# Kernel optimization log

Hardware: AMD Instinct MI355X
Metric: run time of the kernel (lower is better)

The kernel has to match this reference:

```python
import jax, jax.numpy as jnp
import numpy as np
import math

B, S, HID = 2, 4096, 2048
H, D, C = 16, 128, 256  # heads, head_dim, chunk (block) size
NC = S // C


def _build_slopes(n):
    # faithful port of MiniMaxText01LinearAttention._build_slope_tensor
    def p2(m):
        start = 2.0 ** (-(2.0 ** (-(math.log2(m) - 3))))
        return [start * (start ** i) for i in range(m)]
    if math.log2(n).is_integer():
        sl = p2(n)
    else:
        cp = 2 ** math.floor(math.log2(n))
        sl = p2(cp) + p2(2 * cp)[0::2][: n - cp]
    return np.asarray(sl, dtype=np.float32).reshape(n, 1, 1)


def setup_inputs() -> dict:
    key = jax.random.key(0)
    k1, k2, k3, k4 = jax.random.split(key, 4)
    x = jax.random.normal(k1, (B, S, HID), dtype=jnp.float32)
    w_qkv = jax.random.normal(k2, (HID, 3 * H * D), dtype=jnp.float32) * 0.02
    w_gate = jax.random.normal(k3, (HID, H * D), dtype=jnp.float32) * 0.02
    w_out = jax.random.normal(k4, (H * D, HID), dtype=jnp.float32) * 0.02
    slopes = jnp.asarray(_build_slopes(H))  # [H,1,1]
    return {"x": x, "w_qkv": w_qkv, "w_gate": w_gate, "w_out": w_out, "slopes": slopes}


def _to_chunks(t):
    # [B,S,H*D] -> [NC,B,H,C,D]
    return (t.reshape(B, S, H, D)
             .transpose(0, 2, 1, 3)          # [B,H,S,D]
             .reshape(B, H, NC, C, D)
             .transpose(2, 0, 1, 3, 4))      # [NC,B,H,C,D]


def _lightning_attn(q, k, v, slopes):
    # q,k,v: [NC,B,H,C,D]; slopes: [H,1,1]
    s = slopes
    pos = jnp.arange(C, dtype=jnp.float32)
    q_decay = jnp.exp(-s * (pos + 1.0).reshape(1, C, 1))        # [H,C,1]
    k_decay = jnp.exp(-s * (C - 1.0 - pos).reshape(1, C, 1))    # [H,C,1]
    idx = pos[:, None] - pos[None, :]                            # [C,C]
    diag_decay = jnp.where(idx >= 0, jnp.exp(-s * idx), 0.0)     # [H,C,C]
    block_decay = jnp.exp(-s * float(C))[None]                   # [1,H,1,1]

    def step(kv, qkv_c):
        qc, kc, vc = qkv_c  # each [B,H,C,D]
        # intra-chunk (causal, decayed)
        scores = jnp.einsum('bhid,bhjd->bhij', qc, kc) * diag_decay
        o = jnp.einsum('bhij,bhjd->bhid', scores, vc)
        # inter-chunk via recurrent state kv: [B,H,D,D]
        o = o + jnp.einsum('bhid,bhde->bhie', qc * q_decay, kv)
        kv = block_decay * kv + jnp.einsum('bhjd,bhje->bhde', kc * k_decay, vc)
        return kv, o

    kv0 = jnp.zeros((B, H, D, D), dtype=q.dtype)
    _, outs = jax.lax.scan(step, kv0, (q, k, v))  # outs: [NC,B,H,C,D]
    return (outs.transpose(1, 2, 0, 3, 4)          # [B,H,NC,C,D]
                .reshape(B, H, S, D)
                .transpose(0, 2, 1, 3)
                .reshape(B, S, H * D))


def reference(x, w_qkv, w_gate, w_out, slopes):
    qkv = jax.nn.silu(x @ w_qkv)                   # act on fused qkv (hidden_act=silu)
    q, k, v = jnp.split(qkv, 3, axis=-1)
    attn = _lightning_attn(_to_chunks(q), _to_chunks(k), _to_chunks(v), slopes)
    gate = jax.nn.sigmoid(x @ w_gate)              # output gate
    return (gate * attn) @ w_out
```

## Files before the change

kernel.cpp:

```cpp
#include <hip/hip_runtime.h>

typedef __bf16 bf16;
typedef __bf16 bf16x8 __attribute__((ext_vector_type(8)));
typedef __bf16 bf16x4 __attribute__((ext_vector_type(4)));
typedef float  f32x4  __attribute__((ext_vector_type(4)));

#define B_   2
#define S_   4096
#define HID_ 2048
#define H_   16
#define D_   128
#define C_   256
#define NC_  16
#define M_   (B_*S_)
#define K_   2048

typedef __attribute__((address_space(1))) const void gas_t;
typedef __attribute__((address_space(3))) void las_t;

__global__ void cvt_kernel(const float* __restrict__ x,
                           const float* __restrict__ wqkv,
                           const float* __restrict__ wgate,
                           const float* __restrict__ wout,
                           bf16* __restrict__ xb, bf16* __restrict__ wT) {
    __shared__ float tile[32][33];
    int bid = blockIdx.x, tid = threadIdx.x;
    if (bid < 8192) {
        int idx = (bid * 256 + tid) * 8;
        float4 f0 = *(const float4*)(x + idx);
        float4 f1 = *(const float4*)(x + idx + 4);
        bf16x8 o;
        o[0] = (bf16)f0.x; o[1] = (bf16)f0.y; o[2] = (bf16)f0.z; o[3] = (bf16)f0.w;
        o[4] = (bf16)f1.x; o[5] = (bf16)f1.y; o[6] = (bf16)f1.z; o[7] = (bf16)f1.w;
        *(bf16x8*)(xb + idx) = o;
        return;
    }
    bid -= 8192;
    int k0 = (bid & 63) * 32, n0 = (bid >> 6) * 32;
    const float* src; int ld, col0;
    if (n0 < 6144)      { src = wqkv;  ld = 6144; col0 = n0; }
    else if (n0 < 8192) { src = wgate; ld = 2048; col0 = n0 - 6144; }
    else                { src = wout;  ld = 2048; col0 = n0 - 8192; }
    int tx = tid & 31, ty = tid >> 5;
#pragma unroll
    for (int i = 0; i < 4; i++) {
        int kk = ty + i * 8;
        tile[kk][tx] = src[(size_t)(k0 + kk) * ld + col0 + tx];
    }
    __syncthreads();
#pragma unroll
    for (int i = 0; i < 4; i++) {
        int nn = ty + i * 8;
        wT[(size_t)(n0 + nn) * K_ + k0 + tx] = (bf16)tile[tx][nn];
    }
}

template <int MODE>
__global__ __launch_bounds__(256) void gemm_kernel(
        const bf16* __restrict__ A, const bf16* __restrict__ Bm,
        bf16* __restrict__ qo, bf16* __restrict__ ko,
        bf16* __restrict__ vo, bf16* __restrict__ go,
        float* __restrict__ out) {
    __shared__ __align__(16) bf16 As[128 * 64];
    __shared__ __align__(16) bf16 Bs[128 * 64];
    const int m0 = blockIdx.x * 128, n0 = blockIdx.y * 128;
    const int tid = threadIdx.x, lane = tid & 63, wid = tid >> 6;
    const int quad = lane >> 4, l15 = lane & 15;
    const int i0w = (wid >> 1) * 64, j0w = (wid & 1) * 64;
    f32x4 acc[4][4] = {};
    const int srow = tid >> 3;
    const int sl = (tid & 7) ^ (srow & 7);
    const bf16* Ag = A  + (size_t)(m0 + srow) * K_ + sl * 8;
    const bf16* Bg = Bm + (size_t)(n0 + srow) * K_ + sl * 8;
    bf16* AsDst = As + tid * 8;
    bf16* BsDst = Bs + tid * 8;
    const int xr = l15 & 7;

    for (int kb = 0; kb < K_; kb += 64) {
#pragma unroll
        for (int r = 0; r < 4; r++) {
            __builtin_amdgcn_global_load_lds((gas_t*)(Ag + kb + (size_t)r * 32 * K_),
                                             (las_t*)(AsDst + r * 2048), 16, 0, 0);
            __builtin_amdgcn_global_load_lds((gas_t*)(Bg + kb + (size_t)r * 32 * K_),
                                             (las_t*)(BsDst + r * 2048), 16, 0, 0);
        }
        __syncthreads();
        bf16x8 af[2][4], bfr[2][4];
#pragma unroll
        for (int s2 = 0; s2 < 2; s2++) {
            const int slot = (s2 * 4 + quad) ^ xr;
#pragma unroll
            for (int t = 0; t < 4; t++) {
                af[s2][t]  = *(const bf16x8*)&As[(i0w + t * 16 + l15) * 64 + slot * 8];
                bfr[s2][t] = *(const bf16x8*)&Bs[(j0w + t * 16 + l15) * 64 + slot * 8];
            }
        }
#pragma unroll
        for (int s2 = 0; s2 < 2; s2++)
#pragma unroll
            for (int ti = 0; ti < 4; ti++)
#pragma unroll
                for (int tj = 0; tj < 4; tj++)
                    acc[ti][tj] = __builtin_amdgcn_mfma_f32_16x16x32_bf16(
                        af[s2][ti], bfr[s2][tj], acc[ti][tj], 0, 0, 0);
        __syncthreads();
    }

    if (MODE == 0) {
        bf16* outb = (n0 < 2048) ? qo : (n0 < 4096) ? ko : (n0 < 6144) ? vo : go;
        const bool silu = (n0 < 6144);
        const int cb = n0 & 2047;
#pragma unroll
        for (int ti = 0; ti < 4; ti++)
#pragma unroll
            for (int tj = 0; tj < 4; tj++)
#pragma unroll
                for (int r = 0; r < 4; r++) {
                    int row = m0 + i0w + ti * 16 + quad * 4 + r;
                    int col = cb + j0w + tj * 16 + l15;
                    float xv = acc[ti][tj][r];
                    float sg = 1.f / (1.f + __expf(-xv));
                    float av = silu ? xv * sg : sg;
                    outb[(size_t)row * 2048 + col] = (bf16)av;
                }
    } else {
#pragma unroll
        for (int ti = 0; ti < 4; ti++)
#pragma unroll
            for (int tj = 0; tj < 4; tj++)
#pragma unroll
                for (int r = 0; r < 4; r++) {
                    int row = m0 + i0w + ti * 16 + quad * 4 + r;
                    int col = n0 + j0w + tj * 16 + l15;
                    out[(size_t)row * 2048 + col] = acc[ti][tj][r];
                }
    }
}

__global__ void transpose_kernel(const bf16* __restrict__ kin,
                                 const bf16* __restrict__ vin,
                                 const float* __restrict__ slopes,
                                 bf16* __restrict__ kT, bf16* __restrict__ vT) {
    __shared__ bf16 tile[64][65];
    int x0 = blockIdx.x * 64, d0 = blockIdx.y * 64;
    int z = blockIdx.z, arr = z >> 5, bh = z & 31, b = bh >> 4, h = bh & 15;
    const bf16* src = arr ? vin : kin;
    bf16* dst = arr ? vT : kT;
    int tx = threadIdx.x, ty = threadIdx.y;
    float fscale = 1.f;
    if (arr == 0)
        fscale = __expf(-slopes[h] * (float)(255 - ((x0 + tx) & 255)));
#pragma unroll
    for (int r = 0; r < 16; r++) {
        int lr = ty * 16 + r;
        tile[lr][tx] = src[(size_t)(b * S_ + x0 + lr) * 2048 + h * 128 + d0 + tx];
    }
    __syncthreads();
#pragma unroll
    for (int r = 0; r < 16; r++) {
        int lr = ty * 16 + r;
        dst[(size_t)(bh * 128 + d0 + lr) * S_ + x0 + tx] =
            (bf16)((float)tile[tx][lr] * fscale);
    }
}

__global__ __launch_bounds__(256) void pass_a_kernel(
        const bf16* __restrict__ kT, const bf16* __restrict__ vT,
        bf16* __restrict__ KVT) {
    int c = blockIdx.x, bh = blockIdx.y;
    int tid = threadIdx.x, lane = tid & 63, wid = tid >> 6;
    int quad = lane >> 4, l15 = lane & 15;
    int e0 = (wid >> 1) * 64, d0 = (wid & 1) * 64;
    const bf16* vb = vT + (size_t)bh * 128 * S_ + c * 256;
    const bf16* kb = kT + (size_t)bh * 128 * S_ + c * 256;
    f32x4 acc[4][4] = {};
    for (int kbs = 0; kbs < 256; kbs += 32) {
        int j0 = kbs + quad * 8;
        bf16x8 af[4], bfr[4];
#pragma unroll
        for (int t = 0; t < 4; t++)
            af[t] = *(const bf16x8*)(vb + (size_t)(e0 + t * 16 + l15) * S_ + j0);
#pragma unroll
        for (int t = 0; t < 4; t++)
            bfr[t] = *(const bf16x8*)(kb + (size_t)(d0 + t * 16 + l15) * S_ + j0);
#pragma unroll
        for (int ti = 0; ti < 4; ti++)
#pragma unroll
            for (int tj = 0; tj < 4; tj++)
                acc[ti][tj] = __builtin_amdgcn_mfma_f32_16x16x32_bf16(
                    af[ti], bfr[tj], acc[ti][tj], 0, 0, 0);
    }
    size_t base = ((size_t)c * 32 + bh) * 16384;
#pragma unroll
    for (int ti = 0; ti < 4; ti++)
#pragma unroll
        for (int tj = 0; tj < 4; tj++)
#pragma unroll
            for (int r = 0; r < 4; r++) {
                int e = e0 + ti * 16 + quad * 4 + r, d = d0 + tj * 16 + l15;
                KVT[base + (size_t)e * 128 + d] = (bf16)acc[ti][tj][r];
            }
}

__global__ void scan_kernel(const bf16* __restrict__ KVT,
                            const float* __restrict__ slopes,
                            bf16* __restrict__ stT) {
    int slice = blockIdx.x, bh = blockIdx.y;
    float s = slopes[bh & 15];
    float bd = __expf(-s * 256.f);
    size_t off = (size_t)slice * 1024 + threadIdx.x * 4;
    float kv0 = 0.f, kv1 = 0.f, kv2 = 0.f, kv3 = 0.f;
    for (int c = 0; c < 16; c++) {
        size_t idx = ((size_t)c * 32 + bh) * 16384 + off;
        bf16x4 st;
        st[0] = (bf16)kv0; st[1] = (bf16)kv1; st[2] = (bf16)kv2; st[3] = (bf16)kv3;
        *(bf16x4*)(stT + idx) = st;
        bf16x4 kvc = *(const bf16x4*)(KVT + idx);
        kv0 = bd * kv0 + (float)kvc[0];
        kv1 = bd * kv1 + (float)kvc[1];
        kv2 = bd * kv2 + (float)kvc[2];
        kv3 = bd * kv3 + (float)kvc[3];
    }
}

__global__ __launch_bounds__(256) void pass_c_kernel(
        const bf16* __restrict__ q, const bf16* __restrict__ kk,
        const bf16* __restrict__ vT, const bf16* __restrict__ stT,
        const bf16* __restrict__ gate, const float* __restrict__ slopes,
        bf16* __restrict__ og) {
    __shared__ __align__(16) bf16 P[256 * 72];
    __shared__ float dtab[257];
    int c = blockIdx.x, bh = blockIdx.y, b = bh >> 4, h = bh & 15;
    int tid = threadIdx.x, lane = tid & 63, wid = tid >> 6;
    int quad = lane >> 4, l15 = lane & 15;
    int i0 = wid * 64;
    float s = slopes[h];
    dtab[tid] = __expf(-s * (float)tid);
    if (tid == 0) dtab[256] = __expf(-s * 256.f);
    __syncthreads();
    const bf16* qb = q  + ((size_t)(b * S_ + c * 256)) * 2048 + h * 128;
    const bf16* kb = kk + ((size_t)(b * S_ + c * 256)) * 2048 + h * 128;
    const bf16* vb = vT + (size_t)bh * 128 * S_ + c * 256;
    const bf16* st = stT + ((size_t)c * 32 + bh) * 16384;
    f32x4 acc[4][8] = {};

    for (int kbs = 0; kbs < 128; kbs += 32) {
        bf16x8 af[4];
#pragma unroll
        for (int t = 0; t < 4; t++)
            af[t] = *(const bf16x8*)(qb + (size_t)(i0 + t * 16 + l15) * 2048 + kbs + quad * 8);
#pragma unroll
        for (int te = 0; te < 8; te++) {
            bf16x8 bfr = *(const bf16x8*)(st + (size_t)(te * 16 + l15) * 128 + kbs + quad * 8);
#pragma unroll
            for (int t = 0; t < 4; t++)
                acc[t][te] = __builtin_amdgcn_mfma_f32_16x16x32_bf16(
                    af[t], bfr, acc[t][te], 0, 0, 0);
        }
    }
#pragma unroll
    for (int t = 0; t < 4; t++) {
        float qd[4];
#pragma unroll
        for (int r = 0; r < 4; r++) qd[r] = dtab[i0 + t * 16 + quad * 4 + r + 1];
#pragma unroll
        for (int te = 0; te < 8; te++)
#pragma unroll
            for (int r = 0; r < 4; r++) acc[t][te][r] *= qd[r];
    }

    for (int jt = 0; jt <= wid; jt++) {
        f32x4 sacc[4][4] = {};
        for (int kbs = 0; kbs < 128; kbs += 32) {
            bf16x8 af[4], bkr[4];
#pragma unroll
            for (int t = 0; t < 4; t++)
                af[t] = *(const bf16x8*)(qb + (size_t)(i0 + t * 16 + l15) * 2048 + kbs + quad * 8);
#pragma unroll
            for (int t = 0; t < 4; t++)
                bkr[t] = *(const bf16x8*)(kb + (size_t)(jt * 64 + t * 16 + l15) * 2048 + kbs + quad * 8);
#pragma unroll
            for (int ti = 0; ti < 4; ti++)
#pragma unroll
                for (int tj = 0; tj < 4; tj++)
                    sacc[ti][tj] = __builtin_amdgcn_mfma_f32_16x16x32_bf16(
                        af[ti], bkr[tj], sacc[ti][tj], 0, 0, 0);
        }
#pragma unroll
        for (int ti = 0; ti < 4; ti++)
#pragma unroll
            for (int tj = 0; tj < 4; tj++)
#pragma unroll
                for (int r = 0; r < 4; r++) {
                    int i = i0 + ti * 16 + quad * 4 + r;
                    int j = jt * 64 + tj * 16 + l15;
                    int diff = i - j;
                    float pv = (diff >= 0) ? sacc[ti][tj][r] * dtab[diff] : 0.f;
                    P[i * 72 + tj * 16 + l15] = (bf16)pv;
                }
#pragma unroll
        for (int k2 = 0; k2 < 64; k2 += 32) {
            bf16x8 af[4];
#pragma unroll
            for (int t = 0; t < 4; t++)
                af[t] = *(const bf16x8*)&P[(i0 + t * 16 + l15) * 72 + k2 + quad * 8];
#pragma unroll
            for (int te = 0; te < 8; te++) {
                bf16x8 bfr = *(const bf16x8*)(vb + (size_t)(te * 16 + l15) * S_ + jt * 64 + k2 + quad * 8);
#pragma unroll
                for (int t = 0; t < 4; t++)
                    acc[t][te] = __builtin_amdgcn_mfma_f32_16x16x32_bf16(
                        af[t], bfr, acc[t][te], 0, 0, 0);
            }
        }
    }

    const bf16* gb = gate + ((size_t)(b * S_ + c * 256)) * 2048 + h * 128;
    bf16* ob = og + ((size_t)(b * S_ + c * 256)) * 2048 + h * 128;
#pragma unroll
    for (int ti = 0; ti < 4; ti++)
#pragma unroll
        for (int te = 0; te < 8; te++)
#pragma unroll
            for (int r = 0; r < 4; r++) {
                int i = i0 + ti * 16 + quad * 4 + r;
                int e = te * 16 + l15;
                float gv = (float)gb[(size_t)i * 2048 + e];
                ob[(size_t)i * 2048 + e] = (bf16)(acc[ti][te][r] * gv);
            }
}

extern "C" void kernel_launch(void* const* d_in, const int* in_sizes, int n_in,
                              void* d_out, int out_size, void* d_ws, size_t ws_size,
                              hipStream_t stream) {
    const float* x      = (const float*)d_in[0];
    const float* wqkv   = (const float*)d_in[1];
    const float* wgate  = (const float*)d_in[2];
    const float* wout   = (const float*)d_in[3];
    const float* slopes = (const float*)d_in[4];
    float* out = (float*)d_out;

    bf16* wT   = (bf16*)d_ws;
    bf16* xb   = wT   + (size_t)10240 * 2048;
    bf16* qb   = xb   + (size_t)8192 * 2048;
    bf16* kbuf = qb   + (size_t)8192 * 2048;
    bf16* vbuf = kbuf + (size_t)8192 * 2048;
    bf16* gbuf = vbuf + (size_t)8192 * 2048;
    bf16* kT   = xb;
    bf16* vT   = (bf16*)d_out;
    bf16* KVT  = vT + (size_t)32 * 128 * 4096;
    bf16* stT  = KVT + (size_t)16 * 32 * 16384;

    cvt_kernel<<<dim3(28672), dim3(256), 0, stream>>>(x, wqkv, wgate, wout, xb, wT);
    gemm_kernel<0><<<dim3(64, 64), dim3(256), 0, stream>>>(
        xb, wT, qb, kbuf, vbuf, gbuf, (float*)nullptr);
    transpose_kernel<<<dim3(64, 2, 64), dim3(64, 4), 0, stream>>>(
        kbuf, vbuf, slopes, kT, vT);
    pass_a_kernel<<<dim3(16, 32), dim3(256), 0, stream>>>(kT, vT, KVT);
    scan_kernel<<<dim3(16, 32), dim3(256), 0, stream>>>(KVT, slopes, stT);
    pass_c_kernel<<<dim3(16, 32), dim3(256), 0, stream>>>(
        qb, kbuf, vT, stT, gbuf, slopes, vbuf);
    gemm_kernel<1><<<dim3(64, 16), dim3(256), 0, stream>>>(
        vbuf, wT + (size_t)8192 * 2048, nullptr, nullptr, nullptr, nullptr, out);
}
```

Measured before the change: 697.4 us.

## Rewrite GEMM as 256x256 tile, 8-wave, double-buffered pipelined kernel

Replaces the 128x128 single-buffered bf16 MFMA GEMM with a 256x256 block tile computed by 512 threads. LDS is double-buffered, and global-to-LDS loads for later k-tiles are interleaved with MFMA phases, using explicit vmcnt waits, barriers and setprio. The larger tile raises data reuse per LDS load and aims to hide load latency behind compute. In exchange, LDS use is higher (128 KB per block), register pressure grows, and there are fewer blocks, which leaves less parallel slack on the output GEMM (256 blocks).

```diff
diff --git a/kernel.cpp b/kernel.cpp
--- a/kernel.cpp
+++ b/kernel.cpp
@@ -55,87 +55,166 @@
     }
 }
 
+#define DSRA(dst, buf, tb) do {                                              \
+    const bf16* _p = &As[buf][wr][0];                                        \
+    _Pragma("unroll")                                                        \
+    for (int _t = 0; _t < 4; _t++) {                                         \
+        const int _r = ((tb) + _t) * 16 + l15;                               \
+        dst[_t][0] = *(const bf16x8*)(_p + _r * 64 + ps0);                   \
+        dst[_t][1] = *(const bf16x8*)(_p + _r * 64 + ps1);                   \
+    }                                                                        \
+} while (0)
+
+#define DSRB(dst, buf, tb) do {                                              \
+    const bf16* _p = &Bs[buf][wch][0];                                       \
+    _Pragma("unroll")                                                        \
+    for (int _t = 0; _t < 2; _t++) {                                         \
+        const int _r = bro + ((tb) + _t) * 16 + l15;                         \
+        dst[_t][0] = *(const bf16x8*)(_p + _r * 64 + ps0);                   \
+        dst[_t][1] = *(const bf16x8*)(_p + _r * 64 + ps1);                   \
+    }                                                                        \
+} while (0)
+
+#define STAGE_A(buf, h, kt) do {                                             \
+    const bf16* _s = Ag + (size_t)(h) * (128 * K_) + (kt) * 64;              \
+    bf16* _d = &As[buf][h][srow * 64 + sslot * 8];                           \
+    __builtin_amdgcn_global_load_lds((gas_t*)_s, (las_t*)_d, 16, 0, 0);      \
+    __builtin_amdgcn_global_load_lds((gas_t*)(_s + (size_t)64 * K_),         \
+                                     (las_t*)(_d + 4096), 16, 0, 0);         \
+} while (0)
+
+#define STAGE_B(buf, h, kt) do {                                             \
+    const bf16* _s = Bg + (size_t)(h) * (128 * K_) + (kt) * 64;              \
+    bf16* _d = &Bs[buf][h][srow * 64 + sslot * 8];                           \
+    __builtin_amdgcn_global_load_lds((gas_t*)_s, (las_t*)_d, 16, 0, 0);      \
+    __builtin_amdgcn_global_load_lds((gas_t*)(_s + (size_t)64 * K_),         \
+                                     (las_t*)(_d + 4096), 16, 0, 0);         \
+} while (0)
+
+#define MM8(afr, bfr, ib, jb) do {                                           \
+    _Pragma("unroll")                                                        \
+    for (int _i = 0; _i < 4; _i++)                                           \
+        _Pragma("unroll")                                                    \
+        for (int _j = 0; _j < 2; _j++)                                       \
+            _Pragma("unroll")                                                \
+            for (int _k = 0; _k < 2; _k++)                                   \
+                acc[(ib) + _i][(jb) + _j] =                                  \
+                    __builtin_amdgcn_mfma_f32_16x16x32_bf16(                 \
+                        afr[_i][_k], bfr[_j][_k],                            \
+                        acc[(ib) + _i][(jb) + _j], 0, 0, 0);                 \
+} while (0)
+
+#define PTAIL(...) do {                                                      \
+    __builtin_amdgcn_s_barrier();                                            \
+    asm volatile("s_waitcnt lgkmcnt(0)" ::: "memory");                       \
+    __builtin_amdgcn_s_setprio(1);                                           \
+    __VA_ARGS__;                                                             \
+    __builtin_amdgcn_s_setprio(0);                                           \
+    __builtin_amdgcn_s_barrier();                                            \
+} while (0)
+
+#define VMC6 asm volatile("s_waitcnt vmcnt(6)" ::: "memory")
+#define VMC0 asm volatile("s_waitcnt vmcnt(0)" ::: "memory")
+
 template <int MODE>
-__global__ __launch_bounds__(256) void gemm_kernel(
+__global__ __launch_bounds__(512, 2) void gemm_kernel(
         const bf16* __restrict__ A, const bf16* __restrict__ Bm,
         bf16* __restrict__ qo, bf16* __restrict__ ko,
         bf16* __restrict__ vo, bf16* __restrict__ go,
         float* __restrict__ out) {
-    __shared__ __align__(16) bf16 As[128 * 64];
-    __shared__ __align__(16) bf16 Bs[128 * 64];
-    const int m0 = blockIdx.x * 128, n0 = blockIdx.y * 128;
+    __shared__ __align__(16) bf16 As[2][2][128 * 64];
+    __shared__ __align__(16) bf16 Bs[2][2][128 * 64];
+    const int m0 = blockIdx.x * 256, n0 = blockIdx.y * 256;
     const int tid = threadIdx.x, lane = tid & 63, wid = tid >> 6;
     const int quad = lane >> 4, l15 = lane & 15;
-    const int i0w = (wid >> 1) * 64, j0w = (wid & 1) * 64;
-    f32x4 acc[4][4] = {};
-    const int srow = tid >> 3;
-    const int sl = (tid & 7) ^ (srow & 7);
-    const bf16* Ag = A  + (size_t)(m0 + srow) * K_ + sl * 8;
-    const bf16* Bg = Bm + (size_t)(n0 + srow) * K_ + sl * 8;
-    bf16* AsDst = As + tid * 8;
-    bf16* BsDst = Bs + tid * 8;
-    const int xr = l15 & 7;
-
-    for (int kb = 0; kb < K_; kb += 64) {
-#pragma unroll
-        for (int r = 0; r < 4; r++) {
-            __builtin_amdgcn_global_load_lds((gas_t*)(Ag + kb + (size_t)r * 32 * K_),
-                                             (las_t*)(AsDst + r * 2048), 16, 0, 0);
-            __builtin_amdgcn_global_load_lds((gas_t*)(Bg + kb + (size_t)r * 32 * K_),
-                                             (las_t*)(BsDst + r * 2048), 16, 0, 0);
-        }
-        __syncthreads();
-        bf16x8 af[2][4], bfr[2][4];
-#pragma unroll
-        for (int s2 = 0; s2 < 2; s2++) {
-            const int slot = (s2 * 4 + quad) ^ xr;
-#pragma unroll
-            for (int t = 0; t < 4; t++) {
-                af[s2][t]  = *(const bf16x8*)&As[(i0w + t * 16 + l15) * 64 + slot * 8];
-                bfr[s2][t] = *(const bf16x8*)&Bs[(j0w + t * 16 + l15) * 64 + slot * 8];
-            }
-        }
-#pragma unroll
-        for (int s2 = 0; s2 < 2; s2++)
-#pragma unroll
-            for (int ti = 0; ti < 4; ti++)
-#pragma unroll
-                for (int tj = 0; tj < 4; tj++)
-                    acc[ti][tj] = __builtin_amdgcn_mfma_f32_16x16x32_bf16(
-                        af[s2][ti], bfr[s2][tj], acc[ti][tj], 0, 0, 0);
-        __syncthreads();
-    }
-
+    const int wr = wid >> 2, wc = wid & 3;
+    const int wch = wc >> 1, bro = (wc & 1) * 64;
+    const int srow = tid >> 3, sslot = tid & 7;
+    const int lcol = (sslot ^ (srow & 7)) * 8;
+    const int ps0 = ((quad)     ^ (l15 & 7)) * 8;
+    const int ps1 = ((quad + 4) ^ (l15 & 7)) * 8;
+    const bf16* Ag = A  + (size_t)(m0 + srow) * K_ + lcol;
+    const bf16* Bg = Bm + (size_t)(n0 + srow) * K_ + lcol;
+
+    f32x4 acc[8][4] = {};
+    bf16x8 aLo[4][2], aHi[4][2], bLo[2][2], bHi[2][2];
+
+    STAGE_A(0, 0, 0); STAGE_A(0, 1, 0);
+    STAGE_B(0, 0, 0); STAGE_B(0, 1, 0);
+    STAGE_B(1, 0, 1); STAGE_B(1, 1, 1);
+    STAGE_A(1, 0, 1);
+    VMC6;
+    __builtin_amdgcn_s_barrier();
+
+#pragma unroll 1
+    for (int it = 0; it < 16; ++it) {
+        const bool last = (it == 15);
+        const int t2 = 2 * it + 2, t3 = 2 * it + 3;
+        DSRA(aLo, 0, 0); DSRB(bLo, 0, 0);
+        STAGE_A(1, 1, 2 * it + 1);
+        PTAIL(MM8(aLo, bLo, 0, 0));
+        DSRB(bHi, 0, 2);
+        PTAIL(MM8(aLo, bHi, 0, 2));
+        DSRA(aHi, 0, 4);
+        if (!last) { STAGE_B(0, 0, t2); STAGE_B(0, 1, t2); }
+        PTAIL(MM8(aHi, bLo, 4, 0));
+        if (!last) STAGE_A(0, 0, t2);
+        if (last) VMC0; else VMC6;
+        PTAIL(MM8(aHi, bHi, 4, 2));
+        DSRA(aLo, 1, 0); DSRB(bLo, 1, 0);
+        if (!last) STAGE_A(0, 1, t2);
+        PTAIL(MM8(aLo, bLo, 0, 0));
+        DSRB(bHi, 1, 2);
+        PTAIL(MM8(aLo, bHi, 0, 2));
+        DSRA(aHi, 1, 4);
+        if (!last) { STAGE_B(1, 0, t3); STAGE_B(1, 1, t3); }
+        PTAIL(MM8(aHi, bLo, 4, 0));
+        if (!last) STAGE_A(1, 0, t3);
+        if (last) VMC0; else VMC6;
+        PTAIL(MM8(aHi, bHi, 4, 2));
+    }
+
+    const int rb = m0 + wr * 128;
     if (MODE == 0) {
         bf16* outb = (n0 < 2048) ? qo : (n0 < 4096) ? ko : (n0 < 6144) ? vo : go;
         const bool silu = (n0 < 6144);
-        const int cb = n0 & 2047;
-#pragma unroll
-        for (int ti = 0; ti < 4; ti++)
+        const int cb = (n0 & 2047) + wc * 64;
+#pragma unroll
+        for (int ti = 0; ti < 8; ti++)
 #pragma unroll
             for (int tj = 0; tj < 4; tj++)
 #pragma unroll
                 for (int r = 0; r < 4; r++) {
-                    int row = m0 + i0w + ti * 16 + quad * 4 + r;
-                    int col = cb + j0w + tj * 16 + l15;
+                    int row = rb + ti * 16 + quad * 4 + r;
+                    int col = cb + tj * 16 + l15;
                     float xv = acc[ti][tj][r];
                     float sg = 1.f / (1.f + __expf(-xv));
                     float av = silu ? xv * sg : sg;
                     outb[(size_t)row * 2048 + col] = (bf16)av;
                 }
     } else {
-#pragma unroll
-        for (int ti = 0; ti < 4; ti++)
+        const int cb = n0 + wc * 64;
+#pragma unroll
+        for (int ti = 0; ti < 8; ti++)
 #pragma unroll
             for (int tj = 0; tj < 4; tj++)
 #pragma unroll
                 for (int r = 0; r < 4; r++) {
-                    int row = m0 + i0w + ti * 16 + quad * 4 + r;
-                    int col = n0 + j0w + tj * 16 + l15;
+                    int row = rb + ti * 16 + quad * 4 + r;
+                    int col = cb + tj * 16 + l15;
                     out[(size_t)row * 2048 + col] = acc[ti][tj][r];
                 }
     }
 }
+
+#undef DSRA
+#undef DSRB
+#undef STAGE_A
+#undef STAGE_B
+#undef MM8
+#undef PTAIL
+#undef VMC6
+#undef VMC0
 
 __global__ void transpose_kernel(const bf16* __restrict__ kin,
                                  const bf16* __restrict__ vin,
@@ -352,7 +431,7 @@
     bf16* stT  = KVT + (size_t)16 * 32 * 16384;
 
     cvt_kernel<<<dim3(28672), dim3(256), 0, stream>>>(x, wqkv, wgate, wout, xb, wT);
-    gemm_kernel<0><<<dim3(64, 64), dim3(256), 0, stream>>>(
+    gemm_kernel<0><<<dim3(32, 32), dim3(512), 0, stream>>>(
         xb, wT, qb, kbuf, vbuf, gbuf, (float*)nullptr);
     transpose_kernel<<<dim3(64, 2, 64), dim3(64, 4), 0, stream>>>(
         kbuf, vbuf, slopes, kT, vT);
@@ -360,6 +439,6 @@
     scan_kernel<<<dim3(16, 32), dim3(256), 0, stream>>>(KVT, slopes, stT);
     pass_c_kernel<<<dim3(16, 32), dim3(256), 0, stream>>>(
         qb, kbuf, vT, stT, gbuf, slopes, vbuf);
-    gemm_kernel<1><<<dim3(64, 16), dim3(256), 0, stream>>>(
+    gemm_kernel<1><<<dim3(32, 8), dim3(512), 0, stream>>>(
         vbuf, wT + (size_t)8192 * 2048, nullptr, nullptr, nullptr, nullptr, out);
 }
```

Result: faster. 640.1 us (-8.2%).
